# Performance work log

Measured on AMD Instinct MI355X. Metric: run time of the kernel, lower is better.

The kernel has to match this reference:

```python
import jax, jax.numpy as jnp
import numpy as np

EPS = 1e-5

def conv1x1(x, w, b):
    # x: [B,Cin,H,W], w: [Cout,Cin], b: [Cout]
    return jnp.einsum('oi,bihw->bohw', w, x) + b[None, :, None, None]

def self_attention(x, qw, qb, kw, kb, vw, vb, fw, fb):
    B, C, H, W = x.shape
    hid = qw.shape[0]
    q = conv1x1(x, qw, qb).reshape(B, hid, H * W).transpose(0, 2, 1)   # [B,HW,hid]
    k = conv1x1(x, kw, kb).reshape(B, hid, H * W)                      # [B,hid,HW]
    v = conv1x1(x, vw, vb).reshape(B, C, H * W)                        # [B,C,HW]
    attn = jax.nn.softmax(jnp.einsum('bnh,bhm->bnm', q, k), axis=-1)   # [B,HW,HW]
    z = jnp.einsum('bnm,bcm->bnc', attn, v)                            # [B,HW,C]
    # faithful to torch .view(B,C,H,W) on contiguous [B,HW,C]: raw reshape, no transpose
    z = z.reshape(B, C, H, W)
    return conv1x1(z * x, fw, fb) + x

def group_norm_per_channel(y, gw, gb):
    # GroupNorm(num_groups == num_channels): per-channel instance norm, biased var
    mean = y.mean(axis=(2, 3), keepdims=True)
    var = ((y - mean) ** 2).mean(axis=(2, 3), keepdims=True)
    yn = (y - mean) * jax.lax.rsqrt(var + EPS)
    return yn * gw[None, :, None, None] + gb[None, :, None, None]

def setup_inputs() -> dict:
    key = jax.random.key(0)
    ks = jax.random.split(key, 32)
    B, C, H, W = 4, 64, 64, 64
    hid, att = 64, 64
    d = {}
    d['x'] = jax.random.normal(ks[0], (B, C, H, W), jnp.float32)
    d['h'] = jax.random.normal(ks[1], (B, hid, H, W), jnp.float32)
    d['c'] = jax.random.normal(ks[2], (B, hid, H, W), jnp.float32)
    i = 3
    for pre, cin in (('ax', C), ('ah', hid)):
        for nm, cout in (('q', att), ('k', att), ('v', cin), ('f', cin)):
            d[f'{pre}_{nm}w'] = jax.random.normal(ks[i], (cout, cin), jnp.float32) * 0.05; i += 1
            d[f'{pre}_{nm}b'] = jax.random.normal(ks[i], (cout,), jnp.float32) * 0.05; i += 1
    d['conv_w'] = jax.random.normal(ks[i], (4 * hid, C + hid, 3, 3), jnp.float32) * 0.05; i += 1
    d['conv_b'] = jax.random.normal(ks[i], (4 * hid,), jnp.float32) * 0.05; i += 1
    d['gn_w'] = jnp.ones((4 * hid,), jnp.float32)
    d['gn_b'] = jnp.zeros((4 * hid,), jnp.float32)
    return d

def reference(x, h, c,
              ax_qw, ax_qb, ax_kw, ax_kb, ax_vw, ax_vb, ax_fw, ax_fb,
              ah_qw, ah_qb, ah_kw, ah_kb, ah_vw, ah_vb, ah_fw, ah_fb,
              conv_w, conv_b, gn_w, gn_b):
    hid = h.shape[1]
    xa = self_attention(x, ax_qw, ax_qb, ax_kw, ax_kb, ax_vw, ax_vb, ax_fw, ax_fb)
    ha = self_attention(h, ah_qw, ah_qb, ah_kw, ah_kb, ah_vw, ah_vb, ah_fw, ah_fb)
    combined = jnp.concatenate([xa, ha], axis=1)
    y = jax.lax.conv_general_dilated(
        combined, conv_w, window_strides=(1, 1), padding=[(1, 1), (1, 1)],
        dimension_numbers=('NCHW', 'OIHW', 'NCHW')) + conv_b[None, :, None, None]
    y = group_norm_per_channel(y, gn_w, gn_b)
    i, f, o, g = jnp.split(y, 4, axis=1)
    i = jax.nn.sigmoid(i); f = jax.nn.sigmoid(f); o = jax.nn.sigmoid(o); g = jnp.tanh(g)
    c_next = f * c + i * g
    h_next = o * jnp.tanh(c_next)
    return jnp.stack([h_next, c_next])  # [2,B,hid,H,W]
```

## Files before the change

kernel.cpp:

```cpp
#include <hip/hip_runtime.h>
#include <hip/hip_bf16.h>


typedef __hip_bfloat16 bf16;
typedef const __hip_bfloat16* bfp;
typedef short bf16x8 __attribute__((ext_vector_type(8)));
typedef short short4v __attribute__((ext_vector_type(4)));
typedef float f32x4 __attribute__((ext_vector_type(4)));
typedef float f32x16 __attribute__((ext_vector_type(16)));
typedef unsigned int u32x4 __attribute__((ext_vector_type(4)));

#define SM_SHIFT 12.0f
#define SM_A  184.66496523378733f
#define SM_B  14034.452417194552f

__device__ __forceinline__ float ldf(const void* p, long i, int f32) {
    return f32 ? ((const float*)p)[i]
               : __bfloat162float(((const bf16*)p)[i]);
}
__device__ __forceinline__ short f2bf(float f) {
    bf16 h = __float2bfloat16(f);
    return *reinterpret_cast<short*>(&h);
}
__device__ __forceinline__ float bfv(short s) {
    unsigned short u = (unsigned short)s;
    return __bfloat162float(*reinterpret_cast<const bf16*>(&u));
}

__device__ __forceinline__ int sniff_f32(const void* xr)
{
    int lane = threadIdx.x & 63;
    unsigned long long v = ((const unsigned long long*)xr)[lane];
    int ok = 0;
#pragma unroll
    for (int i = 0; i < 4; ++i) {
        int e = (int)((v >> (16 * i + 7)) & 0xFF);
        ok += (e >= 100 && e <= 141);
    }
    ok += __shfl_xor(ok, 1, 64);
    ok += __shfl_xor(ok, 2, 64);
    ok += __shfl_xor(ok, 4, 64);
    ok += __shfl_xor(ok, 8, 64);
    ok += __shfl_xor(ok, 16, 64);
    ok += __shfl_xor(ok, 32, 64);
    return ok < 200;
}

__global__ __launch_bounds__(256) void qkv_kernel(
    const void* __restrict__ Xx, const void* __restrict__ Xh,
    const void* __restrict__ qwx, const void* __restrict__ qbx,
    const void* __restrict__ kwx, const void* __restrict__ kbx,
    const void* __restrict__ vwx, const void* __restrict__ vbx,
    const void* __restrict__ qwh, const void* __restrict__ qbh,
    const void* __restrict__ kwh, const void* __restrict__ kbh,
    const void* __restrict__ vwh, const void* __restrict__ vbh,
    bf16* __restrict__ Qx, bf16* __restrict__ Kx, bf16* __restrict__ Vtx,
    bf16* __restrict__ Qh, bf16* __restrict__ Kh, bf16* __restrict__ Vth,
    const void* __restrict__ cw, bf16* __restrict__ Wt,
    float* __restrict__ gacc, int qkvN)
{
    int bx = blockIdx.x;
    int tid = threadIdx.x;
    int f32 = sniff_f32(Xx);
    if (bx >= qkvN) {
        if (bx == qkvN) {
            for (int j = 0; j < 8; ++j)
                gacc[tid * 8 + j] = 0.f;
        }
        int wi = (bx - qkvN) * 256 + tid;
        int tap = wi >> 15;
        int rem = wi & 32767;
        int oc = rem >> 7, ic = rem & 127;
        Wt[wi] = __float2bfloat16(ldf(cw, ((long)oc * 128 + ic) * 9 + tap, f32));
        return;
    }
    __shared__ __align__(16) short xt[64][72];
    __shared__ __align__(16) short wq[64][72];
    __shared__ __align__(16) short wk[64][72];
    __shared__ __align__(16) short wv[64][72];
    int ab  = (bx >> 8) & 1;
    int idx = bx & 255;
    int b = idx >> 6;
    int n0 = (idx & 63) * 64;
    int wave = tid >> 6, lane = tid & 63;
    int q = lane >> 4, l15 = lane & 15;

    const void* X = ab ? Xh : Xx;
    const void* qw = ab ? qwh : qwx; const void* qb = ab ? qbh : qbx;
    const void* kw = ab ? kwh : kwx; const void* kb = ab ? kbh : kbx;
    const void* vw = ab ? vwh : vwx; const void* vb = ab ? vbh : vbx;
    short* Qg  = (short*)(ab ? Qh  : Qx)  + (long)b * 262144;
    short* Kg  = (short*)(ab ? Kh  : Kx)  + (long)b * 262144;
    short* Vtg = (short*)(ab ? Vth : Vtx) + (long)b * 262144;

    if (!f32) {
        const short* q16 = (const short*)qw;
        const short* k16 = (const short*)kw;
        const short* v16 = (const short*)vw;
        for (int rep = 0; rep < 2; ++rep) {
            int j8 = (rep * 256 + tid) * 8;
            *(bf16x8*)&wq[j8 >> 6][j8 & 63] = *(const bf16x8*)(q16 + j8);
            *(bf16x8*)&wk[j8 >> 6][j8 & 63] = *(const bf16x8*)(k16 + j8);
            *(bf16x8*)&wv[j8 >> 6][j8 & 63] = *(const bf16x8*)(v16 + j8);
        }
    } else {
        for (int rep = 0; rep < 16; ++rep) {
            int j = rep * 256 + tid;
            int i = j >> 6, cc = j & 63;
            wq[i][cc] = f2bf(((const float*)qw)[j]);
            wk[i][cc] = f2bf(((const float*)kw)[j]);
            wv[i][cc] = f2bf(((const float*)vw)[j]);
        }
    }
    long xbase = (long)b * 262144;
    if (!f32) {
        const short* X16 = (const short*)X;
        for (int rep = 0; rep < 2; ++rep) {
            int c = rep * 32 + (tid >> 3);
            int p8 = (tid & 7) * 8;
            bf16x8 v = *(const bf16x8*)(X16 + xbase + (long)c * 4096 + n0 + p8);
#pragma unroll
            for (int j = 0; j < 8; ++j) xt[p8 + j][c] = v[j];
        }
    } else {
        for (int rep = 0; rep < 16; ++rep) {
            int c = rep * 4 + (tid >> 6);
            int p = tid & 63;
            xt[p][c] = f2bf(ldf(X, xbase + (long)c * 4096 + n0 + p, f32));
        }
    }
    __syncthreads();

    bf16x8 a0 = *(const bf16x8*)&xt[wave * 16 + l15][q * 8];
    bf16x8 a1 = *(const bf16x8*)&xt[wave * 16 + l15][32 + q * 8];

    for (int ct = 0; ct < 4; ++ct) {
        bf16x8 bq0 = *(const bf16x8*)&wq[ct * 16 + l15][q * 8];
        bf16x8 bq1 = *(const bf16x8*)&wq[ct * 16 + l15][32 + q * 8];
        f32x4 z = (f32x4){0.f, 0.f, 0.f, 0.f};
        z = __builtin_amdgcn_mfma_f32_16x16x32_bf16(a0, bq0, z, 0, 0, 0);
        z = __builtin_amdgcn_mfma_f32_16x16x32_bf16(a1, bq1, z, 0, 0, 0);
        float bias = ldf(qb, ct * 16 + l15, f32);
        for (int reg = 0; reg < 4; ++reg)
            Qg[(long)(n0 + wave * 16 + q * 4 + reg) * 64 + ct * 16 + l15] =
                f2bf(z[reg] + bias);
    }
    for (int ct = 0; ct < 4; ++ct) {
        bf16x8 bk0 = *(const bf16x8*)&wk[ct * 16 + l15][q * 8];
        bf16x8 bk1 = *(const bf16x8*)&wk[ct * 16 + l15][32 + q * 8];
        f32x4 z = (f32x4){0.f, 0.f, 0.f, 0.f};
        z = __builtin_amdgcn_mfma_f32_16x16x32_bf16(a0, bk0, z, 0, 0, 0);
        z = __builtin_amdgcn_mfma_f32_16x16x32_bf16(a1, bk1, z, 0, 0, 0);
        float bias = ldf(kb, ct * 16 + l15, f32);
        for (int reg = 0; reg < 4; ++reg)
            Kg[(long)(n0 + wave * 16 + q * 4 + reg) * 64 + ct * 16 + l15] =
                f2bf(z[reg] + bias);
    }
    bf16x8 av0 = *(const bf16x8*)&wv[wave * 16 + l15][q * 8];
    bf16x8 av1 = *(const bf16x8*)&wv[wave * 16 + l15][32 + q * 8];
    for (int ct = 0; ct < 4; ++ct) {
        bf16x8 bx0 = *(const bf16x8*)&xt[ct * 16 + l15][q * 8];
        bf16x8 bx1 = *(const bf16x8*)&xt[ct * 16 + l15][32 + q * 8];
        f32x4 z = (f32x4){0.f, 0.f, 0.f, 0.f};
        z = __builtin_amdgcn_mfma_f32_16x16x32_bf16(av0, bx0, z, 0, 0, 0);
        z = __builtin_amdgcn_mfma_f32_16x16x32_bf16(av1, bx1, z, 0, 0, 0);
        for (int reg = 0; reg < 4; ++reg) {
            int c_out = wave * 16 + q * 4 + reg;
            float bias = ldf(vb, c_out, f32);
            Vtg[(long)c_out * 4096 + n0 + ct * 16 + l15] = f2bf(z[reg] + bias);
        }
    }
}

__global__ __launch_bounds__(512, 4) void attn_kernel(
    bfp Qx, bfp Kx, bfp Vtx,
    const void* __restrict__ Xx, const void* __restrict__ fwx,
    const void* __restrict__ fbx, bf16* __restrict__ outx,
    bfp Qh, bfp Kh, bfp Vth,
    const void* __restrict__ Xh, const void* __restrict__ fwh,
    const void* __restrict__ fbh, bf16* __restrict__ outh)
{
    __shared__ __align__(16) short smem[32768];

    int tid = threadIdx.x;
    int wave = tid >> 6, lane = tid & 63;
    int l31 = lane & 31, hi = lane >> 5;
    int nh = wave >> 2, mq = wave & 3;
    int bid = blockIdx.x;
    int ab, b, hrow;
    if (gridDim.x == 512) {
        int abb = bid & 7;
        ab = abb >> 2; b = abb & 3;
        hrow = bid >> 3;
    } else {
        ab = 0; b = bid & 3;
        hrow = bid >> 2;
    }
    int f32 = sniff_f32(Xx);

    const short* Qb  = (const short*)(ab ? Qh  : Qx)  + (long)b * 262144;
    const short* Kb  = (const short*)(ab ? Kh  : Kx)  + (long)b * 262144;
    const short* Vtb = (const short*)(ab ? Vth : Vtx) + (long)b * 262144;
    const void* X  = ab ? Xh  : Xx;
    const void* fw = ab ? fwh : fwx;
    const void* fb = ab ? fbh : fbx;
    bf16* out = ab ? outh : outx;
    long xbase = (long)b * 262144;

    int cnq = nh * 32 + l31;
    long nq = (long)cnq * 64 + hrow;
    bf16x8 aq[4];
#pragma unroll
    for (int kc = 0; kc < 4; ++kc)
        aq[kc] = *(const bf16x8*)(Qb + nq * 64 + kc * 16 + hi * 8);

    f32x16 acc[2];
    acc[0] = (f32x16)(0.0f); acc[1] = (f32x16)(0.0f);
    f32x16 acc_l = (f32x16)(0.0f);
    const short ONE = 0x3F80;
    const bf16x8 ones = {ONE, ONE, ONE, ONE, ONE, ONE, ONE, ONE};

    int krow = mq * 32 + l31;
    int swk = ((krow >> 1) ^ (krow >> 4)) & 7;
    int cR0 = l31, cR1 = 32 + l31;
    int kv0 = (cR0 ^ (cR0 >> 3)) & 7;
    int kv1 = (cR1 ^ (cR1 >> 3)) & 7;

    int r0 = tid >> 3, r1 = r0 + 64;
    int g = tid & 7;
    int sr0 = (r0 & 51) | ((r0 & 4) << 1) | ((r0 & 8) >> 1);
    int sr1 = sr0 + 64;
    int gk0 = (g ^ (((sr0 >> 1) ^ (sr0 >> 4)) & 7)) << 3;
    int gk1 = (g ^ (((sr1 >> 1) ^ (sr1 >> 4)) & 7)) << 3;
    int cV = r0;
    int gv = (g ^ ((cV ^ (cV >> 3)) & 7)) << 3;

    bf16x8 pk0 = *(const bf16x8*)(Kb + (long)r0 * 64 + g * 8);
    bf16x8 pk1 = *(const bf16x8*)(Kb + (long)r1 * 64 + g * 8);
    bf16x8 pv0 = *(const bf16x8*)(Vtb + (long)cV * 4096 + g * 8);
    bf16x8 pv1 = *(const bf16x8*)(Vtb + (long)cV * 4096 + 64 + g * 8);

    for (int mt = 0; mt < 32; ++mt) {
        int buf = mt & 1;
        short* ksw = smem + buf * 8192;
        short* vsw = smem + 16384 + buf * 8192;
        *(bf16x8*)(ksw + sr0 * 64 + gk0)     = pk0;
        *(bf16x8*)(ksw + sr1 * 64 + gk1)     = pk1;
        *(bf16x8*)(vsw + cV * 128 + gv)      = pv0;
        *(bf16x8*)(vsw + cV * 128 + gv + 64) = pv1;
        __syncthreads();
        if (mt + 1 < 32) {
            long m = (long)(mt + 1) * 128;
            pk0 = *(const bf16x8*)(Kb + (m + r0) * 64 + g * 8);
            pk1 = *(const bf16x8*)(Kb + (m + r1) * 64 + g * 8);
            pv0 = *(const bf16x8*)(Vtb + (long)cV * 4096 + m + g * 8);
            pv1 = *(const bf16x8*)(Vtb + (long)cV * 4096 + m + 64 + g * 8);
        }
        const short* ksb  = smem + buf * 8192;
        const short* vtsb = smem + 16384 + buf * 8192;

        f32x16 s = (f32x16)(0.0f);
        const short* kbase = ksb + krow * 64;
#pragma unroll
        for (int kc = 0; kc < 4; ++kc) {
            bf16x8 ak = *(const bf16x8*)(kbase + (((kc * 2 + hi) ^ swk) << 3));
            s = __builtin_amdgcn_mfma_f32_32x32x16_bf16(ak, aq[kc], s, 0, 0, 0);
        }

        unsigned P32[8];
#pragma unroll
        for (int i = 0; i < 8; ++i) {
            unsigned b0 = (unsigned)fmaxf(fmaf(s[2 * i],     SM_A, SM_B), 0.f);
            unsigned b1 = (unsigned)fmaxf(fmaf(s[2 * i + 1], SM_A, SM_B), 0.f);
            P32[i] = b0 | (b1 << 16);
        }
        u32x4 B0v = (u32x4){P32[0], P32[1], P32[2], P32[3]};
        u32x4 B1v = (u32x4){P32[4], P32[5], P32[6], P32[7]};
        bf16x8 bp0 = __builtin_bit_cast(bf16x8, B0v);
        bf16x8 bp1 = __builtin_bit_cast(bf16x8, B1v);

        acc_l = __builtin_amdgcn_mfma_f32_32x32x16_bf16(ones, bp0, acc_l, 0, 0, 0);
        acc_l = __builtin_amdgcn_mfma_f32_32x32x16_bf16(ones, bp1, acc_l, 0, 0, 0);

#pragma unroll
        for (int mc = 0; mc < 2; ++mc) {
            bf16x8 bp = mc ? bp1 : bp0;
            int qch = mq * 4 + mc * 2 + hi;
            bf16x8 av0 = *(const bf16x8*)(
                vtsb + cR0 * 128 + ((qch ^ kv0) << 3));
            bf16x8 av1 = *(const bf16x8*)(
                vtsb + cR1 * 128 + ((qch ^ kv1) << 3));
            acc[0] = __builtin_amdgcn_mfma_f32_32x32x16_bf16(av0, bp, acc[0], 0, 0, 0);
            acc[1] = __builtin_amdgcn_mfma_f32_32x32x16_bf16(av1, bp, acc[1], 0, 0, 0);
        }
    }

    float l_acc = acc_l[0];

    float* fs = (float*)smem;
    float* fl = (float*)smem + 8192;
    short* fwt_s = smem + 16896;
    short* o_lds = smem + 21504;
    short* at_s  = smem;

    __syncthreads();
    if (hi == 0) fl[nh * 128 + mq * 32 + l31] = l_acc;
    if (mq == 1 || mq == 3) {
        int L = mq >> 1;
#pragma unroll
        for (int ch = 0; ch < 2; ++ch)
#pragma unroll
            for (int r = 0; r < 16; ++r) {
                int c = ch * 32 + (r & 3) + ((r >> 2) << 3) + (hi << 2);
                fs[L * 4096 + nh * 2048 + c * 32 + l31] = acc[ch][r];
            }
    }
    if (!f32) {
        int j8 = tid * 8;
        *(bf16x8*)(fwt_s + (j8 >> 6) * 72 + (j8 & 63)) =
            *(const bf16x8*)((const short*)fw + j8);
    } else {
#pragma unroll
        for (int jj = 0; jj < 8; ++jj) {
            int j = tid * 8 + jj;
            fwt_s[(j >> 6) * 72 + (j & 63)] = f2bf(((const float*)fw)[j]);
        }
    }
    __syncthreads();
    if (mq == 0 || mq == 2) {
        int L = mq >> 1;
#pragma unroll
        for (int ch = 0; ch < 2; ++ch)
#pragma unroll
            for (int r = 0; r < 16; ++r) {
                int c = ch * 32 + (r & 3) + ((r >> 2) << 3) + (hi << 2);
                acc[ch][r] += fs[L * 4096 + nh * 2048 + c * 32 + l31];
            }
    }
    __syncthreads();
    if (mq == 2) {
#pragma unroll
        for (int ch = 0; ch < 2; ++ch)
#pragma unroll
            for (int r = 0; r < 16; ++r) {
                int c = ch * 32 + (r & 3) + ((r >> 2) << 3) + (hi << 2);
                fs[nh * 2048 + c * 32 + l31] = acc[ch][r];
            }
    }
    __syncthreads();
    if (mq == 0) {
        float l_tot = fl[nh * 128 + l31]      + fl[nh * 128 + 32 + l31]
                    + fl[nh * 128 + 64 + l31] + fl[nh * 128 + 96 + l31];
        float iln = 1.f / l_tot;
        short* orow = o_lds + cnq * 68;
#pragma unroll
        for (int ch = 0; ch < 2; ++ch)
#pragma unroll
            for (int rq = 0; rq < 4; ++rq) {
                short4v o4;
#pragma unroll
                for (int j = 0; j < 4; ++j) {
                    int r = rq * 4 + j;
                    int c = ch * 32 + (r & 3) + ((r >> 2) << 3) + (hi << 2);
                    o4[j] = f2bf((acc[ch][r] +
                                  fs[nh * 2048 + c * 32 + l31]) * iln);
                }
                *(short4v*)(orow + ch * 32 + rq * 8 + hi * 4) = o4;
            }
    }
    __syncthreads();
    {
        int cn = tid >> 3;
        int w8 = (tid & 7) * 8;
        if (!f32) {
            bf16x8 xv = *(const bf16x8*)(
                (const short*)X + xbase + (long)cn * 4096 + hrow * 64 + w8);
#pragma unroll
            for (int j = 0; j < 8; ++j)
                at_s[(w8 + j) * 78 + cn] =
                    f2bf(bfv(o_lds[cn * 68 + w8 + j]) * bfv(xv[j]));
        } else {
#pragma unroll
            for (int j = 0; j < 8; ++j)
                at_s[(w8 + j) * 78 + cn] =
                    f2bf(bfv(o_lds[cn * 68 + w8 + j]) *
                         ((const float*)X)[xbase + (long)cn * 4096 + hrow * 64 + w8 + j]);
        }
    }
    __syncthreads();
    {
        int q = lane >> 4, l15 = lane & 15;
        int w4 = wave & 3;
        int ntb = (wave >> 2) * 2;
        bf16x8 a0 = *(const bf16x8*)(fwt_s + (w4 * 16 + l15) * 72 + q * 8);
        bf16x8 a1 = *(const bf16x8*)(fwt_s + (w4 * 16 + l15) * 72 + 32 + q * 8);
        short* outp = (short*)out;
        for (int nt = ntb; nt < ntb + 2; ++nt) {
            bf16x8 b0 = *(const bf16x8*)(at_s + (nt * 16 + l15) * 78 + q * 8);
            bf16x8 b1 = *(const bf16x8*)(at_s + (nt * 16 + l15) * 78 + 32 + q * 8);
            f32x4 z = (f32x4){0.f, 0.f, 0.f, 0.f};
            z = __builtin_amdgcn_mfma_f32_16x16x32_bf16(a0, b0, z, 0, 0, 0);
            z = __builtin_amdgcn_mfma_f32_16x16x32_bf16(a1, b1, z, 0, 0, 0);
            int w = nt * 16 + l15;
            short4v o4;
            for (int reg = 0; reg < 4; ++reg) {
                int o = w4 * 16 + q * 4 + reg;
                float v = z[reg] + ldf(fb, o, f32) +
                          ldf(X, xbase + (long)o * 4096 + hrow * 64 + w, f32);
                o4[reg] = f2bf(v);
            }
            *(short4v*)(outp + (((long)(b * 64 + hrow) * 64 + w) * 64
                                + w4 * 16 + q * 4)) = o4;
        }
    }
}

__global__ __launch_bounds__(256) void conv3x3_kernel(
    bfp xa, bfp ha, bfp Wt, const void* __restrict__ cb,
    bf16* __restrict__ y, float* __restrict__ gacc,
    const void* __restrict__ xraw)
{
    __shared__ __align__(16) short in_s[3][66][136];
    int f32 = sniff_f32(xraw);
    int bx = blockIdx.x;
    int b = bx >> 7;
    int rem = bx & 127;
    int h = rem >> 1;
    int halfoc = rem & 1;
    int tid = threadIdx.x;
    int wave = tid >> 6, lane = tid & 63;
    int q = lane >> 4, l15 = lane & 15;

    const short* xab = (const short*)xa + (long)b * 262144;
    const short* hab = (const short*)ha + (long)b * 262144;
    const bf16x8 zv = {0, 0, 0, 0, 0, 0, 0, 0};
    for (int r = 0; r < 3; ++r) {
        int gy = h + r - 1;
        bool valid = (gy >= 0) && (gy < 64);
        for (int s = 0; s < 2; ++s) {
            int strip = s * 256 + tid;
            int w = strip >> 3;
            int c8 = (strip & 7) * 8;
            bf16x8 vx = zv, vh = zv;
            if (valid) {
                vx = *(const bf16x8*)(xab + ((long)gy * 64 + w) * 64 + c8);
                vh = *(const bf16x8*)(hab + ((long)gy * 64 + w) * 64 + c8);
            }
            *(bf16x8*)&in_s[r][w + 1][c8]      = vx;
            *(bf16x8*)&in_s[r][w + 1][64 + c8] = vh;
        }
    }
    if (tid < 96) {
        int r = tid / 32;
        int rest = tid % 32;
        int col = (rest & 1) ? 65 : 0;
        int c8 = (rest >> 1) * 8;
        *(bf16x8*)&in_s[r][col][c8] = zv;
    }
    __syncthreads();

    int oc0 = halfoc * 128 + wave * 32;
    f32x4 acc[2][4];
    for (int mt = 0; mt < 2; ++mt)
        for (int nt = 0; nt < 4; ++nt)
            acc[mt][nt] = (f32x4){0.f, 0.f, 0.f, 0.f};

    const short* Wb = (const short*)Wt;
    for (int tap = 0; tap < 9; ++tap) {
        int dy = tap / 3, dx = tap - dy * 3;
        for (int kc = 0; kc < 4; ++kc) {
            bf16x8 afrag[2];
            for (int mt = 0; mt < 2; ++mt)
                afrag[mt] = *(const bf16x8*)(
                    Wb + ((long)tap * 256 + oc0 + mt * 16 + l15) * 128 + kc * 32 + q * 8);
            for (int nt = 0; nt < 4; ++nt) {
                bf16x8 bfrag = *(const bf16x8*)&in_s[dy][nt * 16 + l15 + dx][kc * 32 + q * 8];
                for (int mt = 0; mt < 2; ++mt)
                    acc[mt][nt] = __builtin_amdgcn_mfma_f32_16x16x32_bf16(
                        afrag[mt], bfrag, acc[mt][nt], 0, 0, 0);
            }
        }
    }

    long ybase = (long)b * 1048576 + (long)h * 64;
    for (int mt = 0; mt < 2; ++mt) {
        for (int reg = 0; reg < 4; ++reg) {
            int oc = oc0 + mt * 16 + q * 4 + reg;
            float bias = ldf(cb, oc, f32);
            float s = 0.f, s2 = 0.f;
            for (int nt = 0; nt < 4; ++nt) {
                float v = acc[mt][nt][reg] + bias;
                ((short*)y)[ybase + (long)oc * 4096 + nt * 16 + l15] = f2bf(v);
                s += v; s2 = fmaf(v, v, s2);
            }
            s  += __shfl_xor(s,  1, 64);  s2 += __shfl_xor(s2, 1, 64);
            s  += __shfl_xor(s,  2, 64);  s2 += __shfl_xor(s2, 2, 64);
            s  += __shfl_xor(s,  4, 64);  s2 += __shfl_xor(s2, 4, 64);
            s  += __shfl_xor(s,  8, 64);  s2 += __shfl_xor(s2, 8, 64);
            if (l15 == 0) {
                atomicAdd(&gacc[b * 256 + oc], s);
                atomicAdd(&gacc[1024 + b * 256 + oc], s2);
            }
        }
    }
}

__global__ __launch_bounds__(256) void gates_kernel(
    bfp y, const float* __restrict__ gacc,
    const void* __restrict__ gw, const void* __restrict__ gb,
    const void* __restrict__ c_in, void* __restrict__ out)
{
    int f32 = sniff_f32(c_in);
    int t = blockIdx.x * 256 + threadIdx.x;
    int b = t >> 15;
    int r = t & 32767;
    int ch = r >> 9;
    int p8 = (r & 511) * 8;
    long ybase = (long)b * 1048576;
    long idx8 = (long)b * 262144 + (long)ch * 4096 + p8;

    float mu[4], rstd[4], gwv[4], gbv[4];
    bf16x8 yv[4];
#pragma unroll
    for (int g = 0; g < 4; ++g) {
        int cc = g * 64 + ch;
        float m = gacc[b * 256 + cc] * (1.f / 4096.f);
        float var = gacc[1024 + b * 256 + cc] * (1.f / 4096.f) - m * m;
        mu[g] = m;
        rstd[g] = rsqrtf(fmaxf(var, 0.f) + 1e-5f);
        gwv[g] = ldf(gw, cc, f32);
        gbv[g] = ldf(gb, cc, f32);
        yv[g] = *(const bf16x8*)((const short*)y + ybase + (long)cc * 4096 + p8);
    }
    float cprev[8];
    if (!f32) {
        bf16x8 cv = *(const bf16x8*)((const short*)c_in + idx8);
#pragma unroll
        for (int j = 0; j < 8; ++j) cprev[j] = bfv(cv[j]);
    } else {
#pragma unroll
        for (int j = 0; j < 8; ++j) cprev[j] = ((const float*)c_in)[idx8 + j];
    }
    bf16x8 hn8, cn8;
    float hnf[8], cnf[8];
#pragma unroll
    for (int j = 0; j < 8; ++j) {
        float v0 = (bfv(yv[0][j]) - mu[0]) * rstd[0] * gwv[0] + gbv[0];
        float v1 = (bfv(yv[1][j]) - mu[1]) * rstd[1] * gwv[1] + gbv[1];
        float v2 = (bfv(yv[2][j]) - mu[2]) * rstd[2] * gwv[2] + gbv[2];
        float v3 = (bfv(yv[3][j]) - mu[3]) * rstd[3] * gwv[3] + gbv[3];
        float ig = 1.f / (1.f + __expf(-v0));
        float fg = 1.f / (1.f + __expf(-v1));
        float og = 1.f / (1.f + __expf(-v2));
        float gg = tanhf(v3);
        float cn = fg * cprev[j] + ig * gg;
        float hn = og * tanhf(cn);
        hn8[j] = f2bf(hn); cn8[j] = f2bf(cn);
        hnf[j] = hn; cnf[j] = cn;
    }
    if (f32) {
        float* o32 = (float*)out;
#pragma unroll
        for (int j = 0; j < 8; ++j) {
            o32[idx8 + j] = hnf[j];
            o32[1048576 + idx8 + j] = cnf[j];
        }
    } else {
        short* o16 = (short*)out;
        *(bf16x8*)(o16 + idx8) = hn8;
        *(bf16x8*)(o16 + 1048576 + idx8) = cn8;
    }
}

extern "C" void kernel_launch(void* const* d_in, const int* in_sizes, int n_in,
                              void* d_out, int out_size, void* d_ws, size_t ws_size,
                              hipStream_t stream)
{
    const void* x = d_in[0]; const void* h = d_in[1]; const void* c = d_in[2];
    const void* ax_qw = d_in[3],  *ax_qb = d_in[4];
    const void* ax_kw = d_in[5],  *ax_kb = d_in[6];
    const void* ax_vw = d_in[7],  *ax_vb = d_in[8];
    const void* ax_fw = d_in[9],  *ax_fb = d_in[10];
    const void* ah_qw = d_in[11], *ah_qb = d_in[12];
    const void* ah_kw = d_in[13], *ah_kb = d_in[14];
    const void* ah_vw = d_in[15], *ah_vb = d_in[16];
    const void* ah_fw = d_in[17], *ah_fb = d_in[18];
    const void* conv_w = d_in[19], *conv_b = d_in[20];
    const void* gn_w = d_in[21],  *gn_b = d_in[22];

    char* wsb = (char*)d_ws;
    auto S = [&](int i) { return wsb + ((unsigned long)i << 21); };
    bool fused = ws_size >= (18ul << 20) + 16384;

    bf16* ha = (bf16*)S(0);
    bf16* Wt = (bf16*)S(1);
    bf16 *Qx, *Kx, *Vtx, *Qh, *Kh, *Vth, *xa, *y;
    char* tail;
    if (fused) {
        Qx = (bf16*)S(2); Kx = (bf16*)S(3); Vtx = (bf16*)S(4);
        Qh = (bf16*)S(5); Kh = (bf16*)S(6); Vth = (bf16*)S(7);
        xa = (bf16*)S(8); y = Qx;
        tail = S(9);
    } else {
        Qx = (bf16*)S(2); Kx = (bf16*)S(3); Vtx = (bf16*)S(4);
        Qh = Qx; Kh = Kx; Vth = Vtx;
        xa = (bf16*)S(6); y = Qx;
        tail = S(7);
    }
    float* gacc = (float*)tail;

    if (fused) {
        qkv_kernel<<<512 + 1152, 256, 0, stream>>>(
            x, h,
            ax_qw, ax_qb, ax_kw, ax_kb, ax_vw, ax_vb,
            ah_qw, ah_qb, ah_kw, ah_kb, ah_vw, ah_vb,
            Qx, Kx, Vtx, Qh, Kh, Vth, conv_w, Wt, gacc, 512);
        attn_kernel<<<512, 512, 0, stream>>>(
            Qx, Kx, Vtx, x, ax_fw, ax_fb, xa,
            Qh, Kh, Vth, h, ah_fw, ah_fb, ha);
    } else {
        qkv_kernel<<<256 + 1152, 256, 0, stream>>>(
            x, x,
            ax_qw, ax_qb, ax_kw, ax_kb, ax_vw, ax_vb,
            ax_qw, ax_qb, ax_kw, ax_kb, ax_vw, ax_vb,
            Qx, Kx, Vtx, Qx, Kx, Vtx, conv_w, Wt, gacc, 256);
        attn_kernel<<<256, 512, 0, stream>>>(
            Qx, Kx, Vtx, x, ax_fw, ax_fb, xa,
            Qx, Kx, Vtx, x, ax_fw, ax_fb, xa);
        qkv_kernel<<<256, 256, 0, stream>>>(
            h, h,
            ah_qw, ah_qb, ah_kw, ah_kb, ah_vw, ah_vb,
            ah_qw, ah_qb, ah_kw, ah_kb, ah_vw, ah_vb,
            Qh, Kh, Vth, Qh, Kh, Vth, conv_w, Wt, gacc, 256);
        attn_kernel<<<256, 512, 0, stream>>>(
            Qh, Kh, Vth, h, ah_fw, ah_fb, ha,
            Qh, Kh, Vth, h, ah_fw, ah_fb, ha);
    }
    conv3x3_kernel<<<512, 256, 0, stream>>>(xa, ha, Wt, conv_b, y, gacc, x);
    gates_kernel<<<512, 256, 0, stream>>>(y, gacc, gn_w, gn_b, c, d_out);
}
```

Baseline: 201.6 us.

## Stage conv weight transpose through LDS and widen conv3x3 blocks to all channels

The conv weight repack now runs in 128 blocks. Each block reads a contiguous 2-output-channel slice with vector loads, transposes it in shared memory, and writes 16-byte vectors. Before, 1152 blocks each did strided scalar gathers. The conv3x3 kernel now uses 512-thread blocks that cover all 256 output channels per row, which halves the block count and halves how often the input halo tile is loaded into LDS. The trade-off is fewer blocks (256) to fill the GPU during the conv, and higher register and LDS pressure per block.

Result: no change. 203.9 us (+1.1%).

```diff
diff --git a/kernel.cpp b/kernel.cpp
--- a/kernel.cpp
+++ b/kernel.cpp
@@ -59,6 +59,10 @@
     const void* __restrict__ cw, bf16* __restrict__ Wt,
     float* __restrict__ gacc, int qkvN)
 {
+    __shared__ __align__(16) short xt[64][72];
+    __shared__ __align__(16) short wq[64][72];
+    __shared__ __align__(16) short wk[64][72];
+    __shared__ __align__(16) short wv[64][72];
     int bx = blockIdx.x;
     int tid = threadIdx.x;
     int f32 = sniff_f32(Xx);
@@ -67,17 +71,40 @@
             for (int j = 0; j < 8; ++j)
                 gacc[tid * 8 + j] = 0.f;
         }
-        int wi = (bx - qkvN) * 256 + tid;
-        int tap = wi >> 15;
-        int rem = wi & 32767;
-        int oc = rem >> 7, ic = rem & 127;
-        Wt[wi] = __float2bfloat16(ldf(cw, ((long)oc * 128 + ic) * 9 + tap, f32));
+        short* tl = &xt[0][0];
+        int t = bx - qkvN;
+        long sbase = (long)t * 2304;
+        if (!f32) {
+            const short* cw16 = (const short*)cw;
+            for (int j = tid; j < 288; j += 256) {
+                bf16x8 v = *(const bf16x8*)(cw16 + sbase + j * 8);
+#pragma unroll
+                for (int e = 0; e < 8; ++e) {
+                    int local = j * 8 + e;
+                    int ocl = local / 1152, rem = local % 1152;
+                    int ic = rem / 9, tap = rem % 9;
+                    tl[ocl * 1152 + tap * 128 + ic] = v[e];
+                }
+            }
+        } else {
+            for (int j = tid; j < 2304; j += 256) {
+                int ocl = j / 1152, rem = j % 1152;
+                int ic = rem / 9, tap = rem % 9;
+                tl[ocl * 1152 + tap * 128 + ic] =
+                    f2bf(((const float*)cw)[sbase + j]);
+            }
+        }
+        __syncthreads();
+        for (int j = tid; j < 288; j += 256) {
+            int d = j * 8;
+            int ocl = d / 1152, rem = d % 1152;
+            int tap = rem / 128, ic0 = rem % 128;
+            bf16x8 v = *(const bf16x8*)(tl + ocl * 1152 + tap * 128 + ic0);
+            *(bf16x8*)((short*)Wt + (long)tap * 32768
+                       + (long)(t * 2 + ocl) * 128 + ic0) = v;
+        }
         return;
     }
-    __shared__ __align__(16) short xt[64][72];
-    __shared__ __align__(16) short wq[64][72];
-    __shared__ __align__(16) short wk[64][72];
-    __shared__ __align__(16) short wv[64][72];
     int ab  = (bx >> 8) & 1;
     int idx = bx & 255;
     int b = idx >> 6;
@@ -415,7 +442,7 @@
     }
 }
 
-__global__ __launch_bounds__(256) void conv3x3_kernel(
+__global__ __launch_bounds__(512) void conv3x3_kernel(
     bfp xa, bfp ha, bfp Wt, const void* __restrict__ cb,
     bf16* __restrict__ y, float* __restrict__ gacc,
     const void* __restrict__ xraw)
@@ -423,10 +450,8 @@
     __shared__ __align__(16) short in_s[3][66][136];
     int f32 = sniff_f32(xraw);
     int bx = blockIdx.x;
-    int b = bx >> 7;
-    int rem = bx & 127;
-    int h = rem >> 1;
-    int halfoc = rem & 1;
+    int b = bx >> 6;
+    int h = bx & 63;
     int tid = threadIdx.x;
     int wave = tid >> 6, lane = tid & 63;
     int q = lane >> 4, l15 = lane & 15;
@@ -437,18 +462,15 @@
     for (int r = 0; r < 3; ++r) {
         int gy = h + r - 1;
         bool valid = (gy >= 0) && (gy < 64);
-        for (int s = 0; s < 2; ++s) {
-            int strip = s * 256 + tid;
-            int w = strip >> 3;
-            int c8 = (strip & 7) * 8;
-            bf16x8 vx = zv, vh = zv;
-            if (valid) {
-                vx = *(const bf16x8*)(xab + ((long)gy * 64 + w) * 64 + c8);
-                vh = *(const bf16x8*)(hab + ((long)gy * 64 + w) * 64 + c8);
-            }
-            *(bf16x8*)&in_s[r][w + 1][c8]      = vx;
-            *(bf16x8*)&in_s[r][w + 1][64 + c8] = vh;
-        }
+        int w = tid >> 3;
+        int c8 = (tid & 7) * 8;
+        bf16x8 vx = zv, vh = zv;
+        if (valid) {
+            vx = *(const bf16x8*)(xab + ((long)gy * 64 + w) * 64 + c8);
+            vh = *(const bf16x8*)(hab + ((long)gy * 64 + w) * 64 + c8);
+        }
+        *(bf16x8*)&in_s[r][w + 1][c8]      = vx;
+        *(bf16x8*)&in_s[r][w + 1][64 + c8] = vh;
     }
     if (tid < 96) {
         int r = tid / 32;
@@ -459,7 +481,7 @@
     }
     __syncthreads();
 
-    int oc0 = halfoc * 128 + wave * 32;
+    int oc0 = wave * 32;
     f32x4 acc[2][4];
     for (int mt = 0; mt < 2; ++mt)
         for (int nt = 0; nt < 4; ++nt)
@@ -610,7 +632,7 @@
     float* gacc = (float*)tail;
 
     if (fused) {
-        qkv_kernel<<<512 + 1152, 256, 0, stream>>>(
+        qkv_kernel<<<512 + 128, 256, 0, stream>>>(
             x, h,
             ax_qw, ax_qb, ax_kw, ax_kb, ax_vw, ax_vb,
             ah_qw, ah_qb, ah_kw, ah_kb, ah_vw, ah_vb,
@@ -619,7 +641,7 @@
             Qx, Kx, Vtx, x, ax_fw, ax_fb, xa,
             Qh, Kh, Vth, h, ah_fw, ah_fb, ha);
     } else {
-        qkv_kernel<<<256 + 1152, 256, 0, stream>>>(
+        qkv_kernel<<<256 + 128, 256, 0, stream>>>(
             x, x,
             ax_qw, ax_qb, ax_kw, ax_kb, ax_vw, ax_vb,
             ax_qw, ax_qb, ax_kw, ax_kb, ax_vw, ax_vb,
@@ -636,6 +658,6 @@
             Qh, Kh, Vth, h, ah_fw, ah_fb, ha,
             Qh, Kh, Vth, h, ah_fw, ah_fb, ha);
     }
-    conv3x3_kernel<<<512, 256, 0, stream>>>(xa, ha, Wt, conv_b, y, gacc, x);
+    conv3x3_kernel<<<256, 512, 0, stream>>>(xa, ha, Wt, conv_b, y, gacc, x);
     gates_kernel<<<512, 256, 0, stream>>>(y, gacc, gn_w, gn_b, c, d_out);
 }
```
